# Kernel tuning notes

Hardware: AMD Instinct MI355X
Metric: run time of the kernel (lower is better)

Reference implementation:

```python
import jax, jax.numpy as jnp
import numpy as np

# DRMamba(dim=64, reverse=True): flip channels, Mamba(d_model=64, d_state=16, d_conv=4, expand=2), flip back.
D_MODEL = 64
D_STATE = 16
D_CONV = 4
EXPAND = 2
D_INNER = EXPAND * D_MODEL  # 128
DT_RANK = (D_MODEL + 15) // 16  # 4
B, H, W = 4, 128, 128


def setup_inputs() -> dict:
    key = jax.random.key(0)
    ks = jax.random.split(key, 9)
    s = lambda k, shape, sc: jax.random.normal(k, shape, jnp.float32) * sc
    x = jax.random.normal(ks[0], (B, D_MODEL, H, W), jnp.float32)
    W_in = s(ks[1], (2 * D_INNER, D_MODEL), 0.05)        # in_proj (no bias)
    conv_w = s(ks[2], (D_INNER, 1, D_CONV), 0.2)         # depthwise causal conv
    conv_b = s(ks[3], (D_INNER,), 0.02)
    W_xproj = s(ks[4], (DT_RANK + 2 * D_STATE, D_INNER), 0.05)  # x_proj (no bias)
    W_dt = s(ks[5], (D_INNER, DT_RANK), 0.1)             # dt_proj
    b_dt = s(ks[6], (D_INNER,), 0.02)
    A_log = jnp.log(jnp.tile(jnp.arange(1.0, D_STATE + 1.0, dtype=jnp.float32), (D_INNER, 1)))
    D_skip = jnp.ones((D_INNER,), jnp.float32)
    W_out = s(ks[7], (D_MODEL, D_INNER), 0.05)           # out_proj (no bias)
    return dict(x=x, W_in=W_in, conv_w=conv_w, conv_b=conv_b, W_xproj=W_xproj,
                W_dt=W_dt, b_dt=b_dt, A_log=A_log, D_skip=D_skip, W_out=W_out)


def _mamba_forward(x, W_in, conv_w, conv_b, W_xproj, W_dt, b_dt, A_log, D_skip, W_out):
    b, c, h, w = x.shape
    xf = x[:, ::-1]                                  # reverse=True: flip channel dim
    seq = xf.reshape(b, c, h * w).transpose(0, 2, 1)  # (b, L, c)
    xz = seq @ W_in.T                                # (b, L, 2*d_inner)
    xi, z = jnp.split(xz, 2, axis=-1)
    # causal depthwise conv along L (pad left d_conv-1), then SiLU
    xc = jax.lax.conv_general_dilated(
        xi.transpose(0, 2, 1), conv_w, (1,), [(D_CONV - 1, 0)],
        dimension_numbers=('NCH', 'OIH', 'NCH'), feature_group_count=D_INNER)
    xc = jax.nn.silu(xc + conv_b[None, :, None]).transpose(0, 2, 1)  # (b, L, d_inner)
    dbl = xc @ W_xproj.T                             # (b, L, dt_rank + 2*d_state)
    dt_r = dbl[..., :DT_RANK]
    Bm = dbl[..., DT_RANK:DT_RANK + D_STATE]          # (b, L, n)
    Cm = dbl[..., DT_RANK + D_STATE:]                 # (b, L, n)
    dt = jax.nn.softplus(dt_r @ W_dt.T + b_dt)        # (b, L, d_inner)
    A = -jnp.exp(A_log)                               # (d_inner, n)

    def step(hst, inp):
        dt_t, B_t, C_t, x_t = inp                     # (b,d),(b,n),(b,n),(b,d)
        dA = jnp.exp(dt_t[..., None] * A)             # (b, d_inner, n)
        hst = dA * hst + (dt_t * x_t)[..., None] * B_t[:, None, :]
        y = jnp.einsum('bdn,bn->bd', hst, C_t)
        return hst, y

    h0 = jnp.zeros((b, D_INNER, D_STATE), x.dtype)
    xs = (dt.transpose(1, 0, 2), Bm.transpose(1, 0, 2), Cm.transpose(1, 0, 2), xc.transpose(1, 0, 2))
    _, ys = jax.lax.scan(step, h0, xs)                # ys: (L, b, d_inner)
    y = ys.transpose(1, 0, 2) + xc * D_skip
    y = y * jax.nn.silu(z)
    out = y @ W_out.T                                 # (b, L, c)
    out = out.transpose(0, 2, 1).reshape(b, c, h, w)
    return out[:, ::-1]                               # flip channels back


def reference(x, W_in, conv_w, conv_b, W_xproj, W_dt, b_dt, A_log, D_skip, W_out):
    return _mamba_forward(x, W_in, conv_w, conv_b, W_xproj, W_dt, b_dt, A_log, D_skip, W_out)
```

## Files before the change

### kernel.cpp

```cpp
#include <hip/hip_runtime.h>
#include <math.h>

#define BATCH 4
#define CM 64
#define LSEQ 16384
#define DIN 128
#define NST 16
#define DTR 4
#define NCHK 256
#define LCHK 64
#define NSC 512

typedef __attribute__((ext_vector_type(8))) short bf16x8;
typedef __attribute__((ext_vector_type(4))) float f32x4;

__device__ __forceinline__ float siluf(float x){ return x / (1.f + __expf(-x)); }
__device__ __forceinline__ unsigned short f2bf_rn(float f){
  unsigned int u = __float_as_uint(f);
  unsigned int r = u + 0x7FFFu + ((u >> 16) & 1u);
  return (unsigned short)(r >> 16);
}
__device__ __forceinline__ float bf2f(unsigned short h){
  return __uint_as_float(((unsigned int)h) << 16);
}
__device__ __forceinline__ float pow_m(float q, int m){
  float q2 = q*q, q4 = q2*q2, q8 = q4*q4;
  float ac = 1.f;
  if (m & 1)  ac *= q;
  if (m & 2)  ac *= q2;
  if (m & 4)  ac *= q4;
  if (m & 8)  ac *= q8;
  if (m & 16) ac *= q8*q8;
  return ac;
}

__global__ __launch_bounds__(256) void k_pre(const float* __restrict__ x, const float* __restrict__ Win,
                                             const float* __restrict__ Wout, const float* __restrict__ Wxp,
                                             unsigned short* __restrict__ WBh, unsigned short* __restrict__ WBl,
                                             float* __restrict__ Wot,
                                             unsigned short* __restrict__ WxpBh, unsigned short* __restrict__ WxpBl,
                                             float* __restrict__ halo){
  __shared__ float Ws[128 * 65];
  int tid = threadIdx.x;
  int bid = blockIdx.x;
  if (bid < 512){
    #pragma unroll
    for (int r = 0; r < 8; ++r){
      int e = r * 256 + tid;
      int d = e >> 4, cq = e & 15;
      float4 v = *(const float4*)(Win + d * CM + cq * 4);
      float* wp = Ws + d * 65 + cq * 4;
      wp[0] = v.x; wp[1] = v.y; wp[2] = v.z; wp[3] = v.w;
    }
    __syncthreads();
    int chunk = bid * 2 + (tid >> 7);
    int d = tid & 127;
    int b  = chunk >> 8;
    int ch = chunk & 255;
    int t0 = ch * LCHK;
    float h0 = 0.f, h1 = 0.f, h2 = 0.f;
    if (ch > 0){
      const float* xb = x + (size_t)b * CM * LSEQ + t0;
      #pragma unroll 8
      for (int c = 0; c < CM; ++c){
        float wv = Ws[d * 65 + (63 - c)];
        const float* xp = xb + (size_t)c * LSEQ;
        h0 += xp[-3] * wv;
        h1 += xp[-2] * wv;
        h2 += xp[-1] * wv;
      }
    }
    float* hp = halo + (size_t)chunk * 384;
    hp[d]       = h0;
    hp[128 + d] = h1;
    hp[256 + d] = h2;
  } else {
    int i = (bid - 512) * 256 + tid;
    if (i < 256 * 64){
      int k = i >> 6, c = i & 63;
      float w = Win[k * CM + (CM - 1 - c)];
      unsigned short h = f2bf_rn(w);
      WBh[i] = h;
      WBl[i] = f2bf_rn(w - bf2f(h));
    }
    int j = i - 256 * 64;
    if (j >= 0 && j < DIN * CM){ int d = j >> 6, c = j & 63; Wot[j] = Wout[c * DIN + d]; }
    int q = j - DIN * CM;
    if (q >= 0 && q < 48 * DIN){
      int o = q >> 7, c = q & 127;
      float w = (o < 36) ? Wxp[o * DIN + c] : 0.f;
      unsigned short h = f2bf_rn(w);
      WxpBh[q] = h;
      WxpBl[q] = f2bf_rn(w - bf2f(h));
    }
  }
}

#define XS_OFF   0
#define BFH_OFF  17408
#define BFL_OFF  25600
#define DL_OFF   33792

__global__ __launch_bounds__(256, 3) void k_mega(const float* __restrict__ x,
                                              const unsigned short* __restrict__ WBh,
                                              const unsigned short* __restrict__ WBl,
                                              const unsigned short* __restrict__ WxpBh,
                                              const unsigned short* __restrict__ WxpBl,
                                              const float* __restrict__ halo,
                                              const float* __restrict__ cw, const float* __restrict__ cb,
                                              const float* __restrict__ Wdt,
                                              const float* __restrict__ bdt, const float* __restrict__ Dsk,
                                              float* __restrict__ z, float2* __restrict__ yp,
                                              float* __restrict__ Cm, float* __restrict__ Pchunk,
                                              float* __restrict__ Hloc){
  __shared__ __align__(16) unsigned char SU[44032];
  float* Xs = (float*)(SU + XS_OFF);
  unsigned short* bfh = (unsigned short*)(SU + BFH_OFF);
  unsigned short* bfl = (unsigned short*)(SU + BFL_OFF);
  float* Xl = (float*)(SU + XS_OFF);
  float* Dl = (float*)(SU + DL_OFF);
  int tid  = threadIdx.x;
  int wave = tid >> 6, lane = tid & 63;
  int l16 = lane & 15, lg = lane >> 4;
  int b  = blockIdx.x >> 8;
  int ch = blockIdx.x & 255;
  int t0g = ch * LCHK;
  size_t T0 = (size_t)b * LSEQ + t0g;

  int d2 = tid & 127;
  int th = tid >> 7;
  float4 cwv  = *(const float4*)(cw + d2 * 4);
  float cbias = cb[d2];
  float4 wr    = *(const float4*)(Wdt + d2 * 4);
  float biasdt = bdt[d2];
  float dsk    = Dsk[d2];
  float hh0 = 0.f, hh1 = 0.f, hh2 = 0.f;
  if (tid < 128){
    const float* hp = halo + (size_t)blockIdx.x * 384;
    hh0 = hp[tid]; hh1 = hp[128 + tid]; hh2 = hp[256 + tid];
  }

  {
    int c  = tid & 63;
    int tq = tid >> 6;
    const float* xc_ = x + ((size_t)b * CM + c) * LSEQ + t0g;
    #pragma unroll
    for (int q = 0; q < 4; ++q){
      int tg = (tq + q * 4) * 4;
      float4 v = *(const float4*)(xc_ + tg);
      Xs[(tg + 0) * 68 + c] = v.x;
      Xs[(tg + 1) * 68 + c] = v.y;
      Xs[(tg + 2) * 68 + c] = v.z;
      Xs[(tg + 3) * 68 + c] = v.w;
    }
  }
  __syncthreads();

  {
    int r  = tid >> 2;
    int cg = (tid & 3) << 4;
    const float* xp = Xs + r * 68 + cg;
    float4 f0 = *(const float4*)(xp);
    float4 f1 = *(const float4*)(xp + 4);
    float4 f2 = *(const float4*)(xp + 8);
    float4 f3 = *(const float4*)(xp + 12);
    float fv[16] = {f0.x,f0.y,f0.z,f0.w, f1.x,f1.y,f1.z,f1.w,
                    f2.x,f2.y,f2.z,f2.w, f3.x,f3.y,f3.z,f3.w};
    int swz = (r & 7) << 4;
    #pragma unroll
    for (int g = 0; g < 2; ++g){
      bf16x8 hi, lo;
      #pragma unroll
      for (int e = 0; e < 8; ++e){
        float v = fv[g*8 + e];
        unsigned short h = f2bf_rn(v);
        hi[e] = (short)h;
        lo[e] = (short)f2bf_rn(v - bf2f(h));
      }
      int cbo = ((cg + g*8) * 2) ^ swz;
      *(bf16x8*)((unsigned char*)bfh + r * 128 + cbo) = hi;
      *(bf16x8*)((unsigned char*)bfl + r * 128 + cbo) = lo;
    }
  }
  __syncthreads();

  f32x4 acc[4][4];
  #pragma unroll
  for (int i = 0; i < 4; ++i)
    #pragma unroll
    for (int j = 0; j < 4; ++j) acc[i][j] = (f32x4){0.f,0.f,0.f,0.f};
  #pragma unroll
  for (int ks = 0; ks < 2; ++ks){
    bf16x8 ah[4], al[4], bh[4], bl[4];
    #pragma unroll
    for (int mi = 0; mi < 4; ++mi){
      int row = mi * 16 + l16;
      int cbo = (ks * 64 + lg * 16) ^ ((row & 7) << 4);
      ah[mi] = *(const bf16x8*)((unsigned char*)bfh + row * 128 + cbo);
      al[mi] = *(const bf16x8*)((unsigned char*)bfl + row * 128 + cbo);
    }
    #pragma unroll
    for (int nj = 0; nj < 4; ++nj){
      size_t off = (size_t)(wave * 64 + nj * 16 + l16) * 64 + ks * 32 + lg * 8;
      bh[nj] = *(const bf16x8*)(WBh + off);
      bl[nj] = *(const bf16x8*)(WBl + off);
    }
    #pragma unroll
    for (int mi = 0; mi < 4; ++mi)
      #pragma unroll
      for (int nj = 0; nj < 4; ++nj){
        acc[mi][nj] = __builtin_amdgcn_mfma_f32_16x16x32_bf16(ah[mi], bh[nj], acc[mi][nj], 0, 0, 0);
        acc[mi][nj] = __builtin_amdgcn_mfma_f32_16x16x32_bf16(ah[mi], bl[nj], acc[mi][nj], 0, 0, 0);
        acc[mi][nj] = __builtin_amdgcn_mfma_f32_16x16x32_bf16(al[mi], bh[nj], acc[mi][nj], 0, 0, 0);
      }
  }
  __syncthreads();

  if (wave < 2){
    #pragma unroll
    for (int nj = 0; nj < 4; ++nj){
      int d = wave * 64 + nj * 16 + l16;
      #pragma unroll
      for (int mi = 0; mi < 4; ++mi){
        int tr = mi * 16 + lg * 4;
        #pragma unroll
        for (int r = 0; r < 4; ++r)
          Xl[(tr + r) * 132 + d] = acc[mi][nj][r];
      }
    }
  }
  __syncthreads();

  float h0, h1, h2;
  if (th == 1){ h0 = Xl[29*132 + d2]; h1 = Xl[30*132 + d2]; h2 = Xl[31*132 + d2]; }
  else        { h0 = hh0; h1 = hh1; h2 = hh2; }
  __syncthreads();
  {
    #pragma unroll
    for (int i = 0; i < 32; i += 4){
      int t = th * 32 + i;
      float x0 = Xl[(t    )*132 + d2];
      float x1 = Xl[(t + 1)*132 + d2];
      float x2 = Xl[(t + 2)*132 + d2];
      float x3 = Xl[(t + 3)*132 + d2];
      float v0 = h0*cwv.x + h1*cwv.y + h2*cwv.z + x0*cwv.w + cbias;
      float v1 = h1*cwv.x + h2*cwv.y + x0*cwv.z + x1*cwv.w + cbias;
      float v2 = h2*cwv.x + x0*cwv.y + x1*cwv.z + x2*cwv.w + cbias;
      float v3 = x0*cwv.x + x1*cwv.y + x2*cwv.z + x3*cwv.w + cbias;
      Xl[(t    )*132 + d2] = siluf(v0);
      Xl[(t + 1)*132 + d2] = siluf(v1);
      Xl[(t + 2)*132 + d2] = siluf(v2);
      Xl[(t + 3)*132 + d2] = siluf(v3);
      h0 = x1; h1 = x2; h2 = x3;
    }
  }
  __syncthreads();

  {
    f32x4 xacc[3];
    #pragma unroll
    for (int nj = 0; nj < 3; ++nj) xacc[nj] = (f32x4){0.f,0.f,0.f,0.f};
    #pragma unroll
    for (int ks = 0; ks < 4; ++ks){
      const float* ap = Xl + (wave * 16 + l16) * 132 + ks * 32 + lg * 8;
      float4 va = *(const float4*)ap;
      float4 vb = *(const float4*)(ap + 4);
      float av[8] = {va.x,va.y,va.z,va.w, vb.x,vb.y,vb.z,vb.w};
      bf16x8 ah, al;
      #pragma unroll
      for (int e = 0; e < 8; ++e){
        unsigned short hh = f2bf_rn(av[e]);
        ah[e] = (short)hh;
        al[e] = (short)f2bf_rn(av[e] - bf2f(hh));
      }
      #pragma unroll
      for (int nj = 0; nj < 3; ++nj){
        size_t off = (size_t)(nj * 16 + l16) * DIN + ks * 32 + lg * 8;
        bf16x8 bh = *(const bf16x8*)(WxpBh + off);
        bf16x8 bl = *(const bf16x8*)(WxpBl + off);
        xacc[nj] = __builtin_amdgcn_mfma_f32_16x16x32_bf16(ah, bh, xacc[nj], 0, 0, 0);
        xacc[nj] = __builtin_amdgcn_mfma_f32_16x16x32_bf16(ah, bl, xacc[nj], 0, 0, 0);
        xacc[nj] = __builtin_amdgcn_mfma_f32_16x16x32_bf16(al, bh, xacc[nj], 0, 0, 0);
      }
    }
    #pragma unroll
    for (int nj = 0; nj < 3; ++nj){
      int o = nj * 16 + l16;
      if (o < 36){
        #pragma unroll
        for (int r = 0; r < 4; ++r)
          Dl[(wave * 16 + lg * 4 + r) * 40 + o] = xacc[nj][r];
      }
    }
  }
  __syncthreads();

  if (wave >= 2){
    #pragma unroll
    for (int nj = 0; nj < 4; ++nj){
      int kz = (wave - 2) * 64 + nj * 16 + l16;
      #pragma unroll
      for (int mi = 0; mi < 4; ++mi){
        size_t rbase = (T0 + mi * 16 + lg * 4) * DIN + kz;
        #pragma unroll
        for (int r = 0; r < 4; ++r)
          z[rbase + (size_t)r * DIN] = acc[mi][nj][r];
      }
    }
  }

  #pragma unroll
  for (int r = 0; r < 4; ++r){
    int e = r * 256 + tid;
    int tt = e >> 4, n = e & 15;
    Cm[(T0 + tt) * NST + n] = Dl[tt * 40 + DTR + NST + n];
  }
  {
    int d  = d2;
    int tb = th * 32;
    float h[16];
    #pragma unroll
    for (int n = 0; n < 16; ++n) h[n] = 0.f;
    float P = 1.f;
    const float* rp0 = Dl + tb * 40;
    float4 dr = *(const float4*)(rp0);
    float4 b0 = *(const float4*)(rp0 + DTR);
    float4 b1 = *(const float4*)(rp0 + DTR + 4);
    float4 b2 = *(const float4*)(rp0 + DTR + 8);
    float4 b3 = *(const float4*)(rp0 + DTR + 12);
    float4 c0 = *(const float4*)(rp0 + DTR + NST);
    float4 c1 = *(const float4*)(rp0 + DTR + NST + 4);
    float4 c2 = *(const float4*)(rp0 + DTR + NST + 8);
    float4 c3 = *(const float4*)(rp0 + DTR + NST + 12);
    float xv = Xl[tb * 132 + d];
    for (int i = 0; i < 32; ++i){
      int t = tb + i;
      float4 drn, b0n, b1n, b2n, b3n, c0n, c1n, c2n, c3n; float xvn;
      if (i + 1 < 32){
        const float* rp = Dl + (t + 1) * 40;
        drn = *(const float4*)(rp);
        b0n = *(const float4*)(rp + DTR);
        b1n = *(const float4*)(rp + DTR + 4);
        b2n = *(const float4*)(rp + DTR + 8);
        b3n = *(const float4*)(rp + DTR + 12);
        c0n = *(const float4*)(rp + DTR + NST);
        c1n = *(const float4*)(rp + DTR + NST + 4);
        c2n = *(const float4*)(rp + DTR + NST + 8);
        c3n = *(const float4*)(rp + DTR + NST + 12);
        xvn = Xl[(t + 1) * 132 + d];
      }
      float dta = fminf(biasdt + dr.x*wr.x + dr.y*wr.y + dr.z*wr.z + dr.w*wr.w, 80.f);
      float e  = __expf(dta);
      float p  = __builtin_amdgcn_rcpf(1.f + e);
      float dtv = -__logf(p);
      float dtx = dtv * xv;
      float p2 = p*p, p4 = p2*p2, p8 = p4*p4;
      float p3 = p2*p, p5 = p4*p, p6 = p4*p2, p7 = p4*p3;
      float p9 = p8*p, p10 = p8*p2, p11 = p8*p3, p12 = p8*p4;
      float p13 = p8*p5, p14 = p8*p6, p15v = p8*p7, p16 = p8*p8;
      h[0]  = p  *h[0]  + dtx*b0.x;  h[1]  = p2 *h[1]  + dtx*b0.y;
      h[2]  = p3 *h[2]  + dtx*b0.z;  h[3]  = p4 *h[3]  + dtx*b0.w;
      h[4]  = p5 *h[4]  + dtx*b1.x;  h[5]  = p6 *h[5]  + dtx*b1.y;
      h[6]  = p7 *h[6]  + dtx*b1.z;  h[7]  = p8 *h[7]  + dtx*b1.w;
      h[8]  = p9 *h[8]  + dtx*b2.x;  h[9]  = p10*h[9]  + dtx*b2.y;
      h[10] = p11*h[10] + dtx*b2.z;  h[11] = p12*h[11] + dtx*b2.w;
      h[12] = p13*h[12] + dtx*b3.x;  h[13] = p14*h[13] + dtx*b3.y;
      h[14] = p15v*h[14] + dtx*b3.z; h[15] = p16*h[15] + dtx*b3.w;
      float yv = h[0]*c0.x + h[1]*c0.y + h[2]*c0.z + h[3]*c0.w
               + h[4]*c1.x + h[5]*c1.y + h[6]*c1.z + h[7]*c1.w
               + h[8]*c2.x + h[9]*c2.y + h[10]*c2.z + h[11]*c2.w
               + h[12]*c3.x + h[13]*c3.y + h[14]*c3.z + h[15]*c3.w;
      P *= p;
      float2 o; o.x = yv + xv * dsk; o.y = P;
      yp[(T0 + t) * DIN + d] = o;
      dr = drn; b0 = b0n; b1 = b1n; b2 = b2n; b3 = b3n;
      c0 = c0n; c1 = c1n; c2 = c2n; c3 = c3n; xv = xvn;
    }
    int sc = ch * 2 + th;
    size_t gbase = ((size_t)sc * (BATCH * DIN) + b * DIN + d) * NST;
    *(float4*)(Hloc + gbase     ) = make_float4(h[0], h[1], h[2], h[3]);
    *(float4*)(Hloc + gbase + 4 ) = make_float4(h[4], h[5], h[6], h[7]);
    *(float4*)(Hloc + gbase + 8 ) = make_float4(h[8], h[9], h[10],h[11]);
    *(float4*)(Hloc + gbase + 12) = make_float4(h[12],h[13],h[14],h[15]);
    Pchunk[(size_t)sc * (BATCH * DIN) + b * DIN + d] = P;
  }
}

__global__ __launch_bounds__(256) void k_scan2(const float* __restrict__ Pchunk, const float* __restrict__ Hloc,
                                               float* __restrict__ H0){
  __shared__ float Bs[NSC * NST];
  __shared__ float Pl[NSC];
  __shared__ float sA[256], sB[256];
  int bd = blockIdx.x;
  int tid = threadIdx.x;
  for (int r = 0; r < 32; ++r){
    int e = r * 256 + tid;
    int c = e >> 4, n = e & 15;
    Bs[e] = Hloc[(size_t)c * (BATCH * DIN * NST) + bd * NST + n];
  }
  Pl[tid]       = Pchunk[(size_t)tid * (BATCH * DIN) + bd];
  Pl[256 + tid] = Pchunk[(size_t)(256 + tid) * (BATCH * DIN) + bd];
  __syncthreads();
  int n = tid & 15, seg = tid >> 4;
  int m = n + 1;
  float a = 1.f, bb = 0.f;
  for (int i = 0; i < 32; ++i){
    int c = seg * 32 + i;
    float ac = pow_m(Pl[c], m);
    bb = ac * bb + Bs[c*16+n];
    a  *= ac;
  }
  sA[tid] = a; sB[tid] = bb;
  __syncthreads();
  for (int off = 1; off < 16; off <<= 1){
    float pa = 1.f, pb = 0.f;
    if (seg >= off){ pa = sA[tid - off*16]; pb = sB[tid - off*16]; }
    float ca = sA[tid], cb = sB[tid];
    __syncthreads();
    sA[tid] = ca * pa; sB[tid] = ca * pb + cb;
    __syncthreads();
  }
  float pb = (seg == 0) ? 0.f : sB[tid - 16];
  for (int i = 0; i < 32; ++i){
    int c = seg * 32 + i;
    H0[(size_t)c * (BATCH * DIN * NST) + bd * NST + n] = pb;
    float ac = pow_m(Pl[c], m);
    pb = ac * pb + Bs[c*16+n];
  }
}

__global__ __launch_bounds__(256) void k_back(const float2* __restrict__ yp, const float* __restrict__ z,
                                              const float* __restrict__ Cm, const float* __restrict__ H0,
                                              const float* __restrict__ Wot, float* __restrict__ out){
  __shared__ float yf[64 * 132];
  int tid = threadIdx.x;
  int b  = blockIdx.x >> 8;
  int ch = blockIdx.x & 255;
  int T0 = b * LSEQ + ch * 64;

  {
    int d  = tid & 127;
    int th = tid >> 7;
    int gb0 = ((2*ch    ) * (BATCH * DIN) + b * DIN + d) * NST;
    int gb1 = ((2*ch + 1) * (BATCH * DIN) + b * DIN + d) * NST;
    float4 a0 = *(const float4*)(H0 + gb0);
    float4 a1 = *(const float4*)(H0 + gb0 + 4);
    float4 a2 = *(const float4*)(H0 + gb0 + 8);
    float4 a3 = *(const float4*)(H0 + gb0 + 12);
    float hvA[16] = {a0.x,a0.y,a0.z,a0.w, a1.x,a1.y,a1.z,a1.w,
                     a2.x,a2.y,a2.z,a2.w, a3.x,a3.y,a3.z,a3.w};
    float4 e0 = *(const float4*)(H0 + gb1);
    float4 e1 = *(const float4*)(H0 + gb1 + 4);
    float4 e2 = *(const float4*)(H0 + gb1 + 8);
    float4 e3 = *(const float4*)(H0 + gb1 + 12);
    float hvB[16] = {e0.x,e0.y,e0.z,e0.w, e1.x,e1.y,e1.z,e1.w,
                     e2.x,e2.y,e2.z,e2.w, e3.x,e3.y,e3.z,e3.w};
    #define BODY(HV, R) { \
      int t = (R) * 2 + th; \
      size_t row = (size_t)(T0 + t) * DIN + d; \
      float2 ypv = yp[row]; \
      float zv = z[row]; \
      size_t cmb = (size_t)(T0 + t) * NST; \
      float4 cva = *(const float4*)(Cm + cmb); \
      float4 cvb = *(const float4*)(Cm + cmb + 4); \
      float4 cvc = *(const float4*)(Cm + cmb + 8); \
      float4 cvd = *(const float4*)(Cm + cmb + 12); \
      float Cv[16] = {cva.x,cva.y,cva.z,cva.w, cvb.x,cvb.y,cvb.z,cvb.w, \
                      cvc.x,cvc.y,cvc.z,cvc.w, cvd.x,cvd.y,cvd.z,cvd.w}; \
      float q = ypv.y; \
      float acc = Cv[15]*HV[15]; \
      _Pragma("unroll") \
      for (int n = 14; n >= 0; --n) acc = acc*q + Cv[n]*HV[n]; \
      acc *= q; \
      float y = ypv.x + acc; \
      yf[t * 132 + d] = y * siluf(zv); }
    for (int r = 0; r < 16; ++r) BODY(hvA, r)
    for (int r = 16; r < 32; ++r) BODY(hvB, r)
    #undef BODY
  }
  __syncthreads();

  {
    int t  = tid & 63;
    int wv = tid >> 6;
    int c0 = __builtin_amdgcn_readfirstlane(wv * 16);
    float acc[16];
    #pragma unroll
    for (int j = 0; j < 16; ++j) acc[j] = 0.f;
    for (int d0 = 0; d0 < DIN; d0 += 4){
      float4 yv = *(const float4*)(yf + t * 132 + d0);
      #pragma unroll
      for (int j = 0; j < 16; ++j){
        acc[j] += yv.x * Wot[(d0    ) * CM + c0 + j]
                + yv.y * Wot[(d0 + 1) * CM + c0 + j]
                + yv.z * Wot[(d0 + 2) * CM + c0 + j]
                + yv.w * Wot[(d0 + 3) * CM + c0 + j];
      }
    }
    int t0g = ch * 64;
    #pragma unroll
    for (int j = 0; j < 16; ++j){
      int c = c0 + j;
      out[(size_t)(b * CM + (CM - 1 - c)) * LSEQ + t0g + t] = acc[j];
    }
  }
}

extern "C" void kernel_launch(void* const* d_in, const int* in_sizes, int n_in,
                              void* d_out, int out_size, void* d_ws, size_t ws_size,
                              hipStream_t stream){
  const float* x    = (const float*)d_in[0];
  const float* Win  = (const float*)d_in[1];
  const float* cw   = (const float*)d_in[2];
  const float* cb   = (const float*)d_in[3];
  const float* Wxp  = (const float*)d_in[4];
  const float* Wdt  = (const float*)d_in[5];
  const float* bdt  = (const float*)d_in[6];
  const float* Dsk  = (const float*)d_in[8];
  const float* Wout = (const float*)d_in[9];
  float* out = (float*)d_out;
  float* ws  = (float*)d_ws;

  const size_t SZ_BIG = (size_t)BATCH * LSEQ * DIN;
  const size_t SZ_BC  = (size_t)BATCH * LSEQ * NST;
  const size_t SZ_SUM = (size_t)NSC * BATCH * DIN * NST;

  float*  z      = ws;
  float2* yp     = (float2*)(z + SZ_BIG);
  float*  Cm     = (float*)(yp + SZ_BIG);
  float*  Pchunk = Cm + SZ_BC;
  float*  Hloc   = Pchunk + (size_t)NSC * BATCH * DIN;
  float*  H0     = Hloc + SZ_SUM;
  float*  Wot    = H0 + SZ_SUM;
  float*  haloA  = Wot + DIN * CM;
  unsigned short* WBh = (unsigned short*)(haloA + (size_t)BATCH * NCHK * 384);
  unsigned short* WBl = WBh + 256 * 64;
  unsigned short* WxpBh = WBl + 256 * 64;
  unsigned short* WxpBl = WxpBh + 48 * DIN;

  k_pre<<<512 + (256*64 + DIN*CM + 48*DIN + 255)/256, 256, 0, stream>>>(
      x, Win, Wout, Wxp, WBh, WBl, Wot, WxpBh, WxpBl, haloA);
  k_mega<<<BATCH * NCHK, 256, 0, stream>>>(x, WBh, WBl, WxpBh, WxpBl, haloA,
                                           cw, cb, Wdt, bdt, Dsk, z, yp, Cm, Pchunk, Hloc);
  k_scan2<<<BATCH * DIN, 256, 0, stream>>>(Pchunk, Hloc, H0);
  k_back<<<BATCH * 256, 256, 0, stream>>>(yp, z, Cm, H0, Wot, out);
}
```

Baseline: 106.5 us.

## Recompute z gate projection in back kernel instead of storing to global

The mega kernel no longer computes the z half of in_proj or writes it to global memory. Its GEMM is split so each of the four waves computes 32 xi columns. The back kernel reloads the x tile, converts it to split bf16, and recomputes z with MFMA into shared memory, then reuses that buffer for the gated output. This removes a 32 MB write plus read of z in exchange for reloading x (8 MB) and redoing the z GEMM in k_back.

```diff
diff --git a/kernel.cpp b/kernel.cpp
--- a/kernel.cpp
+++ b/kernel.cpp
@@ -110,7 +110,7 @@
                                               const float* __restrict__ cw, const float* __restrict__ cb,
                                               const float* __restrict__ Wdt,
                                               const float* __restrict__ bdt, const float* __restrict__ Dsk,
-                                              float* __restrict__ z, float2* __restrict__ yp,
+                                              float2* __restrict__ yp,
                                               float* __restrict__ Cm, float* __restrict__ Pchunk,
                                               float* __restrict__ Hloc){
   __shared__ __align__(16) unsigned char SU[44032];
@@ -184,14 +184,14 @@
   }
   __syncthreads();
 
-  f32x4 acc[4][4];
+  f32x4 acc[4][2];
   #pragma unroll
   for (int i = 0; i < 4; ++i)
     #pragma unroll
-    for (int j = 0; j < 4; ++j) acc[i][j] = (f32x4){0.f,0.f,0.f,0.f};
+    for (int j = 0; j < 2; ++j) acc[i][j] = (f32x4){0.f,0.f,0.f,0.f};
   #pragma unroll
   for (int ks = 0; ks < 2; ++ks){
-    bf16x8 ah[4], al[4], bh[4], bl[4];
+    bf16x8 ah[4], al[4], bh[2], bl[2];
     #pragma unroll
     for (int mi = 0; mi < 4; ++mi){
       int row = mi * 16 + l16;
@@ -200,15 +200,15 @@
       al[mi] = *(const bf16x8*)((unsigned char*)bfl + row * 128 + cbo);
     }
     #pragma unroll
-    for (int nj = 0; nj < 4; ++nj){
-      size_t off = (size_t)(wave * 64 + nj * 16 + l16) * 64 + ks * 32 + lg * 8;
+    for (int nj = 0; nj < 2; ++nj){
+      size_t off = (size_t)(wave * 32 + nj * 16 + l16) * 64 + ks * 32 + lg * 8;
       bh[nj] = *(const bf16x8*)(WBh + off);
       bl[nj] = *(const bf16x8*)(WBl + off);
     }
     #pragma unroll
     for (int mi = 0; mi < 4; ++mi)
       #pragma unroll
-      for (int nj = 0; nj < 4; ++nj){
+      for (int nj = 0; nj < 2; ++nj){
         acc[mi][nj] = __builtin_amdgcn_mfma_f32_16x16x32_bf16(ah[mi], bh[nj], acc[mi][nj], 0, 0, 0);
         acc[mi][nj] = __builtin_amdgcn_mfma_f32_16x16x32_bf16(ah[mi], bl[nj], acc[mi][nj], 0, 0, 0);
         acc[mi][nj] = __builtin_amdgcn_mfma_f32_16x16x32_bf16(al[mi], bh[nj], acc[mi][nj], 0, 0, 0);
@@ -216,10 +216,10 @@
   }
   __syncthreads();
 
-  if (wave < 2){
-    #pragma unroll
-    for (int nj = 0; nj < 4; ++nj){
-      int d = wave * 64 + nj * 16 + l16;
+  {
+    #pragma unroll
+    for (int nj = 0; nj < 2; ++nj){
+      int d = wave * 32 + nj * 16 + l16;
       #pragma unroll
       for (int mi = 0; mi < 4; ++mi){
         int tr = mi * 16 + lg * 4;
@@ -294,20 +294,6 @@
     }
   }
   __syncthreads();
-
-  if (wave >= 2){
-    #pragma unroll
-    for (int nj = 0; nj < 4; ++nj){
-      int kz = (wave - 2) * 64 + nj * 16 + l16;
-      #pragma unroll
-      for (int mi = 0; mi < 4; ++mi){
-        size_t rbase = (T0 + mi * 16 + lg * 4) * DIN + kz;
-        #pragma unroll
-        for (int r = 0; r < 4; ++r)
-          z[rbase + (size_t)r * DIN] = acc[mi][nj][r];
-      }
-    }
-  }
 
   #pragma unroll
   for (int r = 0; r < 4; ++r){
@@ -429,14 +415,104 @@
   }
 }
 
-__global__ __launch_bounds__(256) void k_back(const float2* __restrict__ yp, const float* __restrict__ z,
+#define BXS_OFF  0
+#define BBH_OFF  17408
+#define BBL_OFF  25600
+__global__ __launch_bounds__(256) void k_back(const float* __restrict__ x,
+                                              const unsigned short* __restrict__ WBh,
+                                              const unsigned short* __restrict__ WBl,
+                                              const float2* __restrict__ yp,
                                               const float* __restrict__ Cm, const float* __restrict__ H0,
                                               const float* __restrict__ Wot, float* __restrict__ out){
-  __shared__ float yf[64 * 132];
+  __shared__ __align__(16) unsigned char SU[33792];
+  float* Xs = (float*)(SU + BXS_OFF);
+  unsigned short* bfh = (unsigned short*)(SU + BBH_OFF);
+  unsigned short* bfl = (unsigned short*)(SU + BBL_OFF);
+  float* zl = (float*)(SU);
   int tid = threadIdx.x;
+  int wave = tid >> 6, lane = tid & 63;
+  int l16 = lane & 15, lg = lane >> 4;
   int b  = blockIdx.x >> 8;
   int ch = blockIdx.x & 255;
-  int T0 = b * LSEQ + ch * 64;
+  int t0g = ch * 64;
+  size_t T0 = (size_t)b * LSEQ + t0g;
+
+  {
+    int c  = tid & 63;
+    int tq = tid >> 6;
+    const float* xc_ = x + ((size_t)b * CM + c) * LSEQ + t0g;
+    #pragma unroll
+    for (int q = 0; q < 4; ++q){
+      int tg = (tq + q * 4) * 4;
+      float4 v = *(const float4*)(xc_ + tg);
+      Xs[(tg + 0) * 68 + c] = v.x;
+      Xs[(tg + 1) * 68 + c] = v.y;
+      Xs[(tg + 2) * 68 + c] = v.z;
+      Xs[(tg + 3) * 68 + c] = v.w;
+    }
+  }
+  __syncthreads();
+
+  {
+    int r  = tid >> 2;
+    int cg = (tid & 3) << 4;
+    const float* xp = Xs + r * 68 + cg;
+    float4 f0 = *(const float4*)(xp);
+    float4 f1 = *(const float4*)(xp + 4);
+    float4 f2 = *(const float4*)(xp + 8);
+    float4 f3 = *(const float4*)(xp + 12);
+    float fv[16] = {f0.x,f0.y,f0.z,f0.w, f1.x,f1.y,f1.z,f1.w,
+                    f2.x,f2.y,f2.z,f2.w, f3.x,f3.y,f3.z,f3.w};
+    int swz = (r & 7) << 4;
+    #pragma unroll
+    for (int g = 0; g < 2; ++g){
+      bf16x8 hi, lo;
+      #pragma unroll
+      for (int e = 0; e < 8; ++e){
+        float v = fv[g*8 + e];
+        unsigned short h = f2bf_rn(v);
+        hi[e] = (short)h;
+        lo[e] = (short)f2bf_rn(v - bf2f(h));
+      }
+      int cbo = ((cg + g*8) * 2) ^ swz;
+      *(bf16x8*)((unsigned char*)bfh + r * 128 + cbo) = hi;
+      *(bf16x8*)((unsigned char*)bfl + r * 128 + cbo) = lo;
+    }
+  }
+  __syncthreads();
+
+  f32x4 zacc[8];
+  #pragma unroll
+  for (int j = 0; j < 8; ++j) zacc[j] = (f32x4){0.f,0.f,0.f,0.f};
+  #pragma unroll
+  for (int ks = 0; ks < 2; ++ks){
+    int row = wave * 16 + l16;
+    int cbo = (ks * 64 + lg * 16) ^ ((row & 7) << 4);
+    bf16x8 ah = *(const bf16x8*)((unsigned char*)bfh + row * 128 + cbo);
+    bf16x8 al = *(const bf16x8*)((unsigned char*)bfl + row * 128 + cbo);
+    #pragma unroll
+    for (int nj = 0; nj < 8; ++nj){
+      size_t off = (size_t)(128 + nj * 16 + l16) * 64 + ks * 32 + lg * 8;
+      bf16x8 bh = *(const bf16x8*)(WBh + off);
+      bf16x8 bl = *(const bf16x8*)(WBl + off);
+      zacc[nj] = __builtin_amdgcn_mfma_f32_16x16x32_bf16(ah, bh, zacc[nj], 0, 0, 0);
+      zacc[nj] = __builtin_amdgcn_mfma_f32_16x16x32_bf16(ah, bl, zacc[nj], 0, 0, 0);
+      zacc[nj] = __builtin_amdgcn_mfma_f32_16x16x32_bf16(al, bh, zacc[nj], 0, 0, 0);
+    }
+  }
+  __syncthreads();
+
+  {
+    #pragma unroll
+    for (int nj = 0; nj < 8; ++nj){
+      int kz = nj * 16 + l16;
+      int tr = wave * 16 + lg * 4;
+      #pragma unroll
+      for (int r = 0; r < 4; ++r)
+        zl[(tr + r) * 132 + kz] = zacc[nj][r];
+    }
+  }
+  __syncthreads();
 
   {
     int d  = tid & 127;
@@ -457,10 +533,10 @@
                      e2.x,e2.y,e2.z,e2.w, e3.x,e3.y,e3.z,e3.w};
     #define BODY(HV, R) { \
       int t = (R) * 2 + th; \
-      size_t row = (size_t)(T0 + t) * DIN + d; \
-      float2 ypv = yp[row]; \
-      float zv = z[row]; \
-      size_t cmb = (size_t)(T0 + t) * NST; \
+      size_t row = T0 + t; \
+      float2 ypv = yp[row * DIN + d]; \
+      float zv = zl[t * 132 + d]; \
+      size_t cmb = row * NST; \
       float4 cva = *(const float4*)(Cm + cmb); \
       float4 cvb = *(const float4*)(Cm + cmb + 4); \
       float4 cvc = *(const float4*)(Cm + cmb + 8); \
@@ -473,7 +549,7 @@
       for (int n = 14; n >= 0; --n) acc = acc*q + Cv[n]*HV[n]; \
       acc *= q; \
       float y = ypv.x + acc; \
-      yf[t * 132 + d] = y * siluf(zv); }
+      zl[t * 132 + d] = y * siluf(zv); }
     for (int r = 0; r < 16; ++r) BODY(hvA, r)
     for (int r = 16; r < 32; ++r) BODY(hvB, r)
     #undef BODY
@@ -488,7 +564,7 @@
     #pragma unroll
     for (int j = 0; j < 16; ++j) acc[j] = 0.f;
     for (int d0 = 0; d0 < DIN; d0 += 4){
-      float4 yv = *(const float4*)(yf + t * 132 + d0);
+      float4 yv = *(const float4*)(zl + t * 132 + d0);
       #pragma unroll
       for (int j = 0; j < 16; ++j){
         acc[j] += yv.x * Wot[(d0    ) * CM + c0 + j]
@@ -497,7 +573,6 @@
                 + yv.w * Wot[(d0 + 3) * CM + c0 + j];
       }
     }
-    int t0g = ch * 64;
     #pragma unroll
     for (int j = 0; j < 16; ++j){
       int c = c0 + j;
@@ -525,8 +600,7 @@
   const size_t SZ_BC  = (size_t)BATCH * LSEQ * NST;
   const size_t SZ_SUM = (size_t)NSC * BATCH * DIN * NST;
 
-  float*  z      = ws;
-  float2* yp     = (float2*)(z + SZ_BIG);
+  float2* yp     = (float2*)ws;
   float*  Cm     = (float*)(yp + SZ_BIG);
   float*  Pchunk = Cm + SZ_BC;
   float*  Hloc   = Pchunk + (size_t)NSC * BATCH * DIN;
@@ -541,7 +615,7 @@
   k_pre<<<512 + (256*64 + DIN*CM + 48*DIN + 255)/256, 256, 0, stream>>>(
       x, Win, Wout, Wxp, WBh, WBl, Wot, WxpBh, WxpBl, haloA);
   k_mega<<<BATCH * NCHK, 256, 0, stream>>>(x, WBh, WBl, WxpBh, WxpBl, haloA,
-                                           cw, cb, Wdt, bdt, Dsk, z, yp, Cm, Pchunk, Hloc);
+                                           cw, cb, Wdt, bdt, Dsk, yp, Cm, Pchunk, Hloc);
   k_scan2<<<BATCH * DIN, 256, 0, stream>>>(Pchunk, Hloc, H0);
-  k_back<<<BATCH * 256, 256, 0, stream>>>(yp, z, Cm, H0, Wot, out);
-}
+  k_back<<<BATCH * 256, 256, 0, stream>>>(x, WBh, WBl, yp, Cm, H0, Wot, out);
+}
```

After: 116.8 us. 1.1x slower.
